# Optimization experiments

Measured on AMD Instinct MI355X. Metric: run time of the kernel, lower is better.

The kernel has to match this reference:

```python
import jax, jax.numpy as jnp
import numpy as np
import math

B, S, D_MODEL, N_HEAD, D_HEAD, D_FFN = 1, 2048, 1024, 16, 64, 4096
EPS = 1e-6


def setup_inputs() -> dict:
    key = jax.random.key(0)
    ks = jax.random.split(key, 10)
    scale = 0.02
    x = jax.random.normal(ks[0], (B, S, D_MODEL), dtype=jnp.float32)
    # RoPE frequencies: freqs_cis[s, i] = exp(1j * s * theta_i), theta_i = 10000^{-2i/d_head}
    half = D_HEAD // 2
    inv_freq = 1.0 / (10000.0 ** (jnp.arange(0, half, dtype=jnp.float32) * 2.0 / D_HEAD))
    angles = jnp.arange(S, dtype=jnp.float32)[:, None] * inv_freq[None, :]  # [S, half]
    freqs_cos = jnp.cos(angles)
    freqs_sin = jnp.sin(angles)
    wq = jax.random.normal(ks[1], (D_MODEL, N_HEAD * D_HEAD), dtype=jnp.float32) * scale
    wk = jax.random.normal(ks[2], (D_MODEL, N_HEAD * D_HEAD), dtype=jnp.float32) * scale
    wv = jax.random.normal(ks[3], (D_MODEL, N_HEAD * D_HEAD), dtype=jnp.float32) * scale
    wo = jax.random.normal(ks[4], (N_HEAD * D_HEAD, D_MODEL), dtype=jnp.float32) * scale
    w1 = jax.random.normal(ks[5], (D_MODEL, D_FFN), dtype=jnp.float32) * scale
    w2 = jax.random.normal(ks[6], (D_FFN, D_MODEL), dtype=jnp.float32) * scale
    w3 = jax.random.normal(ks[7], (D_MODEL, D_FFN), dtype=jnp.float32) * scale
    attn_norm_w = jnp.ones((D_MODEL,), dtype=jnp.float32)
    ffn_norm_w = jnp.ones((D_MODEL,), dtype=jnp.float32)
    return {"x": x, "freqs_cos": freqs_cos, "freqs_sin": freqs_sin,
            "wq": wq, "wk": wk, "wv": wv, "wo": wo,
            "w1": w1, "w2": w2, "w3": w3,
            "attn_norm_w": attn_norm_w, "ffn_norm_w": ffn_norm_w}


def _rmsnorm(x, w):
    xf = x.astype(jnp.float32)
    inv = jax.lax.rsqrt(jnp.mean(xf * xf, axis=-1, keepdims=True) + EPS)
    return (xf * inv).astype(x.dtype) * w


def _rope(t, cos, sin):
    # t: [B, S, H, D]; treat last dim as interleaved (even, odd) complex pairs
    b, s, h, d = t.shape
    tr = t.astype(jnp.float32).reshape(b, s, h, d // 2, 2)
    te, to = tr[..., 0], tr[..., 1]
    c = cos[None, :, None, :]
    sn = sin[None, :, None, :]
    out = jnp.stack([te * c - to * sn, te * sn + to * c], axis=-1)
    return out.reshape(b, s, h, d).astype(t.dtype)


def reference(x, freqs_cos, freqs_sin, wq, wk, wv, wo, w1, w2, w3, attn_norm_w, ffn_norm_w):
    bsz, seqlen, _ = x.shape
    # --- attention sub-block ---
    hin = _rmsnorm(x, attn_norm_w)
    q = (hin @ wq).reshape(bsz, seqlen, N_HEAD, D_HEAD)
    k = (hin @ wk).reshape(bsz, seqlen, N_HEAD, D_HEAD)
    v = (hin @ wv).reshape(bsz, seqlen, N_HEAD, D_HEAD)
    q = _rope(q, freqs_cos, freqs_sin)
    k = _rope(k, freqs_cos, freqs_sin)
    # [B, H, S, S] scores, softmax in fp32 (no causal mask in original)
    scores = jnp.einsum('bqhd,bkhd->bhqk', q, k) / math.sqrt(D_HEAD)
    probs = jax.nn.softmax(scores.astype(jnp.float32), axis=-1).astype(q.dtype)
    attn = jnp.einsum('bhqk,bkhd->bqhd', probs, v).reshape(bsz, seqlen, N_HEAD * D_HEAD)
    h = x + attn @ wo
    # --- SwiGLU FFN sub-block ---
    f = _rmsnorm(h, ffn_norm_w)
    ffn = (jax.nn.silu(f @ w1) * (f @ w3)) @ w2
    return h + ffn
```

## Files before the change

kernel.cpp:

```cpp
#include <hip/hip_runtime.h>
#include <stdint.h>
#include <stddef.h>

using bf16x8 = __attribute__((ext_vector_type(8))) __bf16;
using f32x4  = __attribute__((ext_vector_type(4))) float;
using f32x16 = __attribute__((ext_vector_type(16))) float;

__device__ __forceinline__ float bf2f(unsigned short u) {
  union { unsigned int i; float f; } v; v.i = ((unsigned int)u) << 16; return v.f;
}
__device__ __forceinline__ unsigned short f2bf(float f) {
  union { float f; unsigned int i; } v; v.f = f;
  unsigned int r = v.i + 0x7fffu + ((v.i >> 16) & 1u);
  return (unsigned short)(r >> 16);
}
__device__ __forceinline__ unsigned short f2bf_trunc(float f) {
  union { float f; unsigned int i; } v; v.f = f;
  return (unsigned short)(v.i >> 16);
}
__device__ __forceinline__ unsigned int pk_trunc(float a, float b) {
  union { float f; unsigned int i; } x, y; x.f = a; y.f = b;
  return (x.i >> 16) | (y.i & 0xffff0000u);
}
__device__ __forceinline__ bf16x8 mk_bf16x8(unsigned int a, unsigned int b,
                                            unsigned int c, unsigned int d) {
  union { unsigned int u[4]; bf16x8 v; } x;
  x.u[0] = a; x.u[1] = b; x.u[2] = c; x.u[3] = d; return x.v;
}
__device__ __forceinline__ void async16(const void* g, void* l) {
  __builtin_amdgcn_global_load_lds(
      (const __attribute__((address_space(1))) unsigned int*)g,
      (__attribute__((address_space(3))) unsigned int*)l, 16, 0, 0);
}

#define S_LEN 2048
#define DMODEL 1024
#define NHEAD 16
#define DHEAD 64
#define DFFN 4096

struct PrepArgs {
  const float *wq, *wk, *wv, *wo, *w1, *w3, *w2, *x, *anw;
  unsigned short *WqkvT, *WoT, *W13I, *W2T, *Hin;
};
__global__ __launch_bounds__(256) void prep_k(PrepArgs a) {
  __shared__ unsigned short tile[64][66];
  __shared__ float red[4];
  const int bid = blockIdx.x;
  const int t = threadIdx.x;

  if (bid < 4096) {
    const float* in;
    unsigned short* out;
    int src_ld, dst_ld, bx, by;
    bool w13 = false;
    int rb = 0;
    if (bid < 1024) {
      int z = bid >> 8, rem = bid & 255;
      bx = rem & 15; by = rem >> 4;
      in = z == 0 ? a.wq : z == 1 ? a.wk : z == 2 ? a.wv : a.wo;
      out = z == 0 ? a.WqkvT : z == 1 ? a.WqkvT + 1048576 : z == 2 ? a.WqkvT + 2097152 : a.WoT;
      src_ld = 1024; dst_ld = 1024;
    } else if (bid < 3072) {
      int r = bid - 1024;
      int z = r >> 10, rem = r & 1023;
      bx = rem & 63; by = rem >> 6;
      in = z ? a.w3 : a.w1;
      out = a.W13I;
      src_ld = 4096; dst_ld = 1024;
      w13 = true; rb = z * 32;
    } else {
      int r = bid - 3072;
      bx = r & 15; by = r >> 4;
      in = a.w2; out = a.W2T;
      src_ld = 1024; dst_ld = 4096;
    }
    const int br = by * 64, bc = bx * 64;
    const int rr = t >> 4, c4 = (t & 15) * 4;
#pragma unroll
    for (int i = 0; i < 4; ++i) {
      int row = rr + i * 16;
      float4 v = *(const float4*)&in[(size_t)(br + row) * src_ld + bc + c4];
      tile[row][c4 + 0] = f2bf(v.x);
      tile[row][c4 + 1] = f2bf(v.y);
      tile[row][c4 + 2] = f2bf(v.z);
      tile[row][c4 + 3] = f2bf(v.w);
    }
    __syncthreads();
    const int x = t >> 2, y16 = (t & 3) * 16;
    int dest = bc + x;
    if (w13) dest = (bc >> 5) * 64 + (x >> 5) * 64 + rb + (x & 31);
#pragma unroll
    for (int i = 0; i < 2; ++i) {
      int y0 = y16 + i * 8;
      ushort4 o0, o1;
      o0.x = tile[y0 + 0][x]; o0.y = tile[y0 + 1][x];
      o0.z = tile[y0 + 2][x]; o0.w = tile[y0 + 3][x];
      o1.x = tile[y0 + 4][x]; o1.y = tile[y0 + 5][x];
      o1.z = tile[y0 + 6][x]; o1.w = tile[y0 + 7][x];
      *(ushort4*)&out[(size_t)dest * dst_ld + br + y0] = o0;
      *(ushort4*)&out[(size_t)dest * dst_ld + br + y0 + 4] = o1;
    }
  } else {
    const int row = bid - 4096;
    const int lane = t & 63, w = t >> 6;
    const float* x = a.x + (size_t)row * DMODEL;
    float xs[4];
    float s = 0.f;
#pragma unroll
    for (int i = 0; i < 4; ++i) {
      xs[i] = x[t * 4 + i];
      s += xs[i] * xs[i];
    }
#pragma unroll
    for (int m = 1; m < 64; m <<= 1) s += __shfl_xor(s, m, 64);
    if (lane == 0) red[w] = s;
    __syncthreads();
    float tot = red[0] + red[1] + red[2] + red[3];
    float inv = rsqrtf(tot * (1.0f / DMODEL) + 1e-6f);
#pragma unroll
    for (int i = 0; i < 4; ++i)
      a.Hin[(size_t)row * DMODEL + t * 4 + i] = f2bf(xs[i] * inv * a.anw[t * 4 + i]);
  }
}

__global__ __launch_bounds__(256) void rope_vtrans_k(
    unsigned short* __restrict__ QKV,
    const float* __restrict__ cosp,
    const float* __restrict__ sinp,
    unsigned short* __restrict__ VtG) {
  __shared__ unsigned short tile[64][66];
  const int bid = blockIdx.x;
  const int t = threadIdx.x;
  if (bid < 4096) {
    int idx = bid * 256 + t;
    int s = idx >> 9;
    int rem = idx & 511;
    int h = rem >> 5;
    int i = rem & 31;
    float c = cosp[s * 32 + i];
    float sn = sinp[s * 32 + i];
    size_t off = (size_t)s * 3072 + h * 64 + 2 * i;
    {
      float e = bf2f(QKV[off]), o = bf2f(QKV[off + 1]);
      QKV[off] = f2bf(e * c - o * sn);
      QKV[off + 1] = f2bf(e * sn + o * c);
    }
    {
      float e = bf2f(QKV[off + 1024]), o = bf2f(QKV[off + 1025]);
      QKV[off + 1024] = f2bf((e * c - o * sn) * 0.125f);
      QKV[off + 1025] = f2bf((e * sn + o * c) * 0.125f);
    }
  } else {
    int r = bid - 4096;
    const int bx = r & 15, by = r >> 4;
    const int br = by * 64, bc = bx * 64;
    const int rr = t >> 4, c4 = (t & 15) * 4;
#pragma unroll
    for (int i = 0; i < 4; ++i) {
      int row = rr + i * 16;
      ushort4 v = *(const ushort4*)&QKV[(size_t)(br + row) * 3072 + 2048 + bc + c4];
      tile[row][c4 + 0] = v.x;
      tile[row][c4 + 1] = v.y;
      tile[row][c4 + 2] = v.z;
      tile[row][c4 + 3] = v.w;
    }
    __syncthreads();
    const int x = t >> 2, y16 = (t & 3) * 16;
#pragma unroll
    for (int i = 0; i < 2; ++i) {
      int y0 = y16 + i * 8;
      ushort4 o0, o1;
      o0.x = tile[y0 + 0][x]; o0.y = tile[y0 + 1][x];
      o0.z = tile[y0 + 2][x]; o0.w = tile[y0 + 3][x];
      o1.x = tile[y0 + 4][x]; o1.y = tile[y0 + 5][x];
      o1.z = tile[y0 + 6][x]; o1.w = tile[y0 + 7][x];
      *(ushort4*)&VtG[(size_t)(bc + x) * 2048 + br + y0] = o0;
      *(ushort4*)&VtG[(size_t)(bc + x) * 2048 + br + y0 + 4] = o1;
    }
  }
}

template <int MODE>
__global__ __launch_bounds__(256) void gemm_bt(
    const unsigned short* __restrict__ A, int lda,
    const unsigned short* __restrict__ BT,
    void* __restrict__ Cout,
    int K, int N) {
  __shared__ unsigned short As[128 * 64];
  __shared__ unsigned short Bs[128 * 64];
  const int t = threadIdx.x;
  const int lane = t & 63;
  const int w = t >> 6;
  const int qr = (w >> 1) * 64, qc = (w & 1) * 64;
  const int l31 = lane & 31, half = lane >> 5;
  const int m0 = blockIdx.y * 128, n0 = blockIdx.x * 128;

  f32x16 acc[2][2] = {};

  int srow[4], scol[4];
#pragma unroll
  for (int p = 0; p < 4; ++p) {
    int off = p * 2048 + t * 8;
    int r = off >> 6;
    srow[p] = r;
    scol[p] = ((((off >> 3) & 7) ^ (r & 7) ^ ((r >> 3) & 3))) * 8;
  }
  const int gsw = (l31 & 7) ^ (l31 >> 3);

  for (int k0 = 0; k0 < K; k0 += 64) {
    __syncthreads();
#pragma unroll
    for (int p = 0; p < 4; ++p) {
      int off = p * 2048 + t * 8;
      async16(A + (size_t)(m0 + srow[p]) * lda + (k0 + scol[p]), &As[off]);
      async16(BT + (size_t)(n0 + srow[p]) * K + (k0 + scol[p]), &Bs[off]);
    }
    __syncthreads();
#pragma unroll
    for (int ks = 0; ks < 4; ++ks) {
      const int ch = ((ks * 2 + half) ^ gsw) * 8;
      bf16x8 a0 = *(const bf16x8*)&As[(qr + l31) * 64 + ch];
      bf16x8 a1 = *(const bf16x8*)&As[(qr + 32 + l31) * 64 + ch];
      bf16x8 b0 = *(const bf16x8*)&Bs[(qc + l31) * 64 + ch];
      bf16x8 b1 = *(const bf16x8*)&Bs[(qc + 32 + l31) * 64 + ch];
      acc[0][0] = __builtin_amdgcn_mfma_f32_32x32x16_bf16(a0, b0, acc[0][0], 0, 0, 0);
      acc[0][1] = __builtin_amdgcn_mfma_f32_32x32x16_bf16(a0, b1, acc[0][1], 0, 0, 0);
      acc[1][0] = __builtin_amdgcn_mfma_f32_32x32x16_bf16(a1, b0, acc[1][0], 0, 0, 0);
      acc[1][1] = __builtin_amdgcn_mfma_f32_32x32x16_bf16(a1, b1, acc[1][1], 0, 0, 0);
    }
  }

  {
    unsigned short* C = (unsigned short*)Cout;
#pragma unroll
    for (int rt = 0; rt < 2; ++rt)
#pragma unroll
      for (int ct = 0; ct < 2; ++ct)
#pragma unroll
        for (int reg = 0; reg < 16; ++reg) {
          int rr = m0 + qr + rt * 32 + (reg & 3) + 8 * (reg >> 2) + 4 * half;
          int cc = n0 + qc + ct * 32 + l31;
          C[(size_t)rr * N + cc] = f2bf(acc[rt][ct][reg]);
        }
  }
}

__device__ __forceinline__ void mfma8(f32x16& c0, f32x16& c1,
                                      const bf16x8 (&a)[2][4],
                                      const bf16x8 (&b)[4]) {
  __builtin_amdgcn_s_setprio(1);
#pragma unroll
  for (int ks = 0; ks < 4; ++ks) {
    c0 = __builtin_amdgcn_mfma_f32_32x32x16_bf16(a[0][ks], b[ks], c0, 0, 0, 0);
    c1 = __builtin_amdgcn_mfma_f32_32x32x16_bf16(a[1][ks], b[ks], c1, 0, 0, 0);
  }
  __builtin_amdgcn_s_setprio(0);
}

__global__ __launch_bounds__(512, 2) void gemm256_silu(
    const unsigned short* __restrict__ A,
    const unsigned short* __restrict__ BT,
    unsigned short* __restrict__ F) {
  __shared__ unsigned short lds[65536];
  const int t = threadIdx.x;
  const int l = t & 63, l31 = l & 31, half = l >> 5;
  const int w = t >> 6;
  const int wm = w >> 2, wn = w & 3;

  const int orig = blockIdx.x;
  const int bx = (orig & 7) * 4 + ((orig >> 3) & 3);
  const int by = orig >> 5;
  const int m0 = by * 256, n0 = bx * 256;

  const int rA = t >> 3;
  const int sc = ((t & 7) ^ ((t >> 3) & 7)) * 8;
  const int lo = t * 8;

#define STAGE_A(h, tile, d)                                                    \
  { async16(A + (size_t)(m0 + (h) * 128 + rA) * 1024 + (tile) * 64 + sc,       \
            &lds[(d) * 32768 + (h) * 8192 + lo]);                              \
    async16(A + (size_t)(m0 + (h) * 128 + 64 + rA) * 1024 + (tile) * 64 + sc,  \
            &lds[(d) * 32768 + (h) * 8192 + 4096 + lo]); }
#define STAGE_B(h, tile, d)                                                    \
  { async16(BT + (size_t)(n0 + (h) * 128 + rA) * 1024 + (tile) * 64 + sc,      \
            &lds[(d) * 32768 + 16384 + (h) * 8192 + lo]);                      \
    async16(BT + (size_t)(n0 + (h) * 128 + 64 + rA) * 1024 + (tile) * 64 + sc, \
            &lds[(d) * 32768 + 16384 + (h) * 8192 + 4096 + lo]); }

  const int arow = wm * 128 + l31;
  const int brow = wn * 64 + l31;
  int kc[4];
#pragma unroll
  for (int ks = 0; ks < 4; ++ks) kc[ks] = ((ks * 2 + half) ^ (l31 & 7)) * 8;

#define LDA(d, mt, ks) (*(const bf16x8*)&lds[(d) * 32768 + (arow + (mt) * 32) * 64 + kc[ks]])
#define LDB(d, nt, ks) (*(const bf16x8*)&lds[(d) * 32768 + 16384 + (brow + (nt) * 32) * 64 + kc[ks]])

  f32x16 acc[4][2] = {};
  bf16x8 afr[2][4], bfr[2][4];

  STAGE_A(0, 0, 0); STAGE_A(1, 0, 0); STAGE_B(0, 0, 0); STAGE_B(1, 0, 0);
  STAGE_A(0, 1, 1); STAGE_A(1, 1, 1);
  asm volatile("s_waitcnt vmcnt(4)" ::: "memory");
  __builtin_amdgcn_s_barrier();

#pragma unroll 1
  for (int i = 0; i < 8; ++i) {
    const int t1 = 2 * i + 1, t2 = 2 * i + 2, t3 = 2 * i + 3;
    const bool more = i < 7;

#pragma unroll
    for (int ks = 0; ks < 4; ++ks) {
      afr[0][ks] = LDA(0, 0, ks);
      afr[1][ks] = LDA(0, 1, ks);
      bfr[0][ks] = LDB(0, 0, ks);
    }
    STAGE_B(0, t1, 1);
    __builtin_amdgcn_s_barrier();
    mfma8(acc[0][0], acc[1][0], afr, bfr[0]);
    __builtin_amdgcn_s_barrier();

#pragma unroll
    for (int ks = 0; ks < 4; ++ks) bfr[1][ks] = LDB(0, 1, ks);
    STAGE_B(1, t1, 1);
    __builtin_amdgcn_s_barrier();
    mfma8(acc[0][1], acc[1][1], afr, bfr[1]);
    __builtin_amdgcn_s_barrier();

#pragma unroll
    for (int ks = 0; ks < 4; ++ks) {
      afr[0][ks] = LDA(0, 2, ks);
      afr[1][ks] = LDA(0, 3, ks);
    }
    if (more) STAGE_B(0, t2, 0);
    __builtin_amdgcn_s_barrier();
    mfma8(acc[2][1], acc[3][1], afr, bfr[1]);
    __builtin_amdgcn_s_barrier();

    if (more) {
      STAGE_B(1, t2, 0);
      STAGE_A(0, t2, 0);
      asm volatile("s_waitcnt vmcnt(8)" ::: "memory");
    } else {
      asm volatile("s_waitcnt vmcnt(2)" ::: "memory");
    }
    __builtin_amdgcn_s_barrier();
    mfma8(acc[2][0], acc[3][0], afr, bfr[0]);
    __builtin_amdgcn_s_barrier();

#pragma unroll
    for (int ks = 0; ks < 4; ++ks) {
      afr[0][ks] = LDA(1, 0, ks);
      afr[1][ks] = LDA(1, 1, ks);
      bfr[0][ks] = LDB(1, 0, ks);
    }
    if (more) {
      STAGE_A(1, t2, 0);
      asm volatile("s_waitcnt vmcnt(8)" ::: "memory");
    } else {
      asm volatile("s_waitcnt vmcnt(0)" ::: "memory");
    }
    __builtin_amdgcn_s_barrier();
    mfma8(acc[0][0], acc[1][0], afr, bfr[0]);
    __builtin_amdgcn_s_barrier();

#pragma unroll
    for (int ks = 0; ks < 4; ++ks) bfr[1][ks] = LDB(1, 1, ks);
    __builtin_amdgcn_s_barrier();
    mfma8(acc[0][1], acc[1][1], afr, bfr[1]);
    __builtin_amdgcn_s_barrier();

#pragma unroll
    for (int ks = 0; ks < 4; ++ks) {
      afr[0][ks] = LDA(1, 2, ks);
      afr[1][ks] = LDA(1, 3, ks);
    }
    __builtin_amdgcn_s_barrier();
    mfma8(acc[2][1], acc[3][1], afr, bfr[1]);
    __builtin_amdgcn_s_barrier();

    if (more) {
      STAGE_A(0, t3, 1);
      STAGE_A(1, t3, 1);
      asm volatile("s_waitcnt vmcnt(4)" ::: "memory");
    } else {
      asm volatile("s_waitcnt vmcnt(0)" ::: "memory");
    }
    __builtin_amdgcn_s_barrier();
    mfma8(acc[2][0], acc[3][0], afr, bfr[0]);
    __builtin_amdgcn_s_barrier();
  }

#undef STAGE_A
#undef STAGE_B
#undef LDA
#undef LDB

  const int ccol = (n0 >> 1) + wn * 32 + l31;
  const int rbase = m0 + wm * 128 + 4 * half;
#pragma unroll
  for (int mt = 0; mt < 4; ++mt)
#pragma unroll
    for (int reg = 0; reg < 16; ++reg) {
      int rr = rbase + mt * 32 + (reg & 3) + 8 * (reg >> 2);
      float a1v = acc[mt][0][reg];
      float a3v = acc[mt][1][reg];
      float f = a1v / (1.f + __expf(-a1v)) * a3v;
      F[(size_t)rr * 4096 + ccol] = f2bf(f);
    }
}

struct PtrPair { float* p0; float* p1; };

__global__ __launch_bounds__(256) void gemm_bt_sk2(
    const unsigned short* __restrict__ A, int lda,
    const unsigned short* __restrict__ BT,
    PtrPair parts, int Kc, int Ktot, int N) {
  __shared__ unsigned short As[128 * 64];
  __shared__ unsigned short Bs[128 * 64];
  const int t = threadIdx.x;
  const int lane = t & 63;
  const int w = t >> 6;
  const int qr = (w >> 1) * 64, qc = (w & 1) * 64;
  const int l31 = lane & 31, half = lane >> 5;
  const int m0 = blockIdx.y * 128, n0 = blockIdx.x * 128;
  const int kb = blockIdx.z * Kc;

  f32x16 acc[2][2] = {};

  int srow[4], scol[4];
#pragma unroll
  for (int p = 0; p < 4; ++p) {
    int off = p * 2048 + t * 8;
    int r = off >> 6;
    srow[p] = r;
    scol[p] = ((((off >> 3) & 7) ^ (r & 7) ^ ((r >> 3) & 3))) * 8;
  }
  const int gsw = (l31 & 7) ^ (l31 >> 3);

  for (int k0 = kb; k0 < kb + Kc; k0 += 64) {
    __syncthreads();
#pragma unroll
    for (int p = 0; p < 4; ++p) {
      int off = p * 2048 + t * 8;
      async16(A + (size_t)(m0 + srow[p]) * lda + (k0 + scol[p]), &As[off]);
      async16(BT + (size_t)(n0 + srow[p]) * Ktot + (k0 + scol[p]), &Bs[off]);
    }
    __syncthreads();
#pragma unroll
    for (int ks = 0; ks < 4; ++ks) {
      const int ch = ((ks * 2 + half) ^ gsw) * 8;
      bf16x8 a0 = *(const bf16x8*)&As[(qr + l31) * 64 + ch];
      bf16x8 a1 = *(const bf16x8*)&As[(qr + 32 + l31) * 64 + ch];
      bf16x8 b0 = *(const bf16x8*)&Bs[(qc + l31) * 64 + ch];
      bf16x8 b1 = *(const bf16x8*)&Bs[(qc + 32 + l31) * 64 + ch];
      acc[0][0] = __builtin_amdgcn_mfma_f32_32x32x16_bf16(a0, b0, acc[0][0], 0, 0, 0);
      acc[0][1] = __builtin_amdgcn_mfma_f32_32x32x16_bf16(a0, b1, acc[0][1], 0, 0, 0);
      acc[1][0] = __builtin_amdgcn_mfma_f32_32x32x16_bf16(a1, b0, acc[1][0], 0, 0, 0);
      acc[1][1] = __builtin_amdgcn_mfma_f32_32x32x16_bf16(a1, b1, acc[1][1], 0, 0, 0);
    }
  }

  float* C = blockIdx.z ? parts.p1 : parts.p0;
#pragma unroll
  for (int rt = 0; rt < 2; ++rt)
#pragma unroll
    for (int ct = 0; ct < 2; ++ct)
#pragma unroll
      for (int reg = 0; reg < 16; ++reg) {
        int rr = m0 + qr + rt * 32 + (reg & 3) + 8 * (reg >> 2) + 4 * half;
        int cc = n0 + qc + ct * 32 + l31;
        C[(size_t)rr * N + cc] = acc[rt][ct][reg];
      }
}

__global__ __launch_bounds__(256) void reduce2_k(
    const float4* __restrict__ P0, const float4* __restrict__ P1,
    const float4* __restrict__ R, float4* __restrict__ Out, int nvec) {
  int i = blockIdx.x * 256 + threadIdx.x;
  if (i >= nvec) return;
  float4 a = P0[i], b = P1[i], r = R[i];
  float4 o;
  o.x = a.x + b.x + r.x;
  o.y = a.y + b.y + r.y;
  o.z = a.z + b.z + r.z;
  o.w = a.w + b.w + r.w;
  Out[i] = o;
}

__global__ __launch_bounds__(256) void reduce_norm_k(
    const float4* __restrict__ P0, const float4* __restrict__ P1,
    const float4* __restrict__ R, float4* __restrict__ Hres,
    const float* __restrict__ W, unsigned short* __restrict__ Hin) {
  const int row = blockIdx.x;
  const int t = threadIdx.x;
  const int lane = t & 63, w = t >> 6;
  const int i = row * 256 + t;
  float4 a = P0[i], b = P1[i], r = R[i];
  float4 h;
  h.x = a.x + b.x + r.x;
  h.y = a.y + b.y + r.y;
  h.z = a.z + b.z + r.z;
  h.w = a.w + b.w + r.w;
  Hres[i] = h;
  float s = h.x * h.x + h.y * h.y + h.z * h.z + h.w * h.w;
#pragma unroll
  for (int m = 1; m < 64; m <<= 1) s += __shfl_xor(s, m, 64);
  __shared__ float red[4];
  if (lane == 0) red[w] = s;
  __syncthreads();
  float tot = red[0] + red[1] + red[2] + red[3];
  float inv = rsqrtf(tot * (1.0f / DMODEL) + 1e-6f);
  ushort4 o;
  o.x = f2bf(h.x * inv * W[t * 4 + 0]);
  o.y = f2bf(h.y * inv * W[t * 4 + 1]);
  o.z = f2bf(h.z * inv * W[t * 4 + 2]);
  o.w = f2bf(h.w * inv * W[t * 4 + 3]);
  *(ushort4*)(Hin + (size_t)row * DMODEL + t * 4) = o;
}

__global__ __launch_bounds__(256) void attn_k(
    const unsigned short* __restrict__ QKV,
    const unsigned short* __restrict__ VtG,
    float* __restrict__ O0, float* __restrict__ O1,
    float* __restrict__ L) {
  const int h = blockIdx.y;
  const int qb = blockIdx.x;
  const int z = blockIdx.z;
  const int t = threadIdx.x;
  const int lane = t & 63;
  const int l31 = lane & 31, half = lane >> 5;
  const int w = t >> 6;
  const int q0 = qb * 128 + w * 32;
  const int kbase = z * 1024;
  const int gsw = (l31 & 7) ^ (l31 >> 3);

  __shared__ unsigned short Kt[2][64 * 64];
  __shared__ unsigned short Vt[2][64 * 64];

  const unsigned short* Kp = QKV + 1024 + h * 64;
  const unsigned short* Vg = VtG + (size_t)h * 64 * 2048;

  bf16x8 qf[4];
#pragma unroll
  for (int ks = 0; ks < 4; ++ks)
    qf[ks] = *(const bf16x8*)(QKV + (size_t)(q0 + l31) * 3072 + h * 64 + ks * 16 + half * 8);

#pragma unroll
  for (int p = 0; p < 2; ++p) {
    int off = p * 2048 + t * 8;
    int r = off >> 6;
    int sc8 = (((off >> 3) & 7) ^ (r & 7) ^ ((r >> 3) & 3)) * 8;
    async16(Kp + (size_t)(kbase + r) * 3072 + sc8, &Kt[0][off]);
    async16(Vg + (size_t)r * 2048 + kbase + sc8, &Vt[0][off]);
  }
  asm volatile("s_waitcnt vmcnt(0)" ::: "memory");
  __syncthreads();

  f32x16 oacc[2] = {};
  float l_r = 0.f;

#pragma unroll 1
  for (int kt = 0; kt < 16; ++kt) {
    const int cur = kt & 1;
    if (kt + 1 < 16) {
      int kb2 = kbase + (kt + 1) * 64;
#pragma unroll
      for (int p = 0; p < 2; ++p) {
        int off = p * 2048 + t * 8;
        int r = off >> 6;
        int sc8 = (((off >> 3) & 7) ^ (r & 7) ^ ((r >> 3) & 3)) * 8;
        async16(Kp + (size_t)(kb2 + r) * 3072 + sc8, &Kt[cur ^ 1][off]);
        async16(Vg + (size_t)r * 2048 + kb2 + sc8, &Vt[cur ^ 1][off]);
      }
    }

    f32x16 st[2] = {};
#pragma unroll
    for (int ks = 0; ks < 4; ++ks) {
      const int ch = ((2 * ks + half) ^ gsw) * 8;
      bf16x8 k0 = *(const bf16x8*)&Kt[cur][l31 * 64 + ch];
      bf16x8 k1 = *(const bf16x8*)&Kt[cur][(32 + l31) * 64 + ch];
      st[0] = __builtin_amdgcn_mfma_f32_32x32x16_bf16(k0, qf[ks], st[0], 0, 0, 0);
      st[1] = __builtin_amdgcn_mfma_f32_32x32x16_bf16(k1, qf[ks], st[1], 0, 0, 0);
    }

    float psum = 0.f;
#pragma unroll
    for (int b = 0; b < 2; ++b)
#pragma unroll
      for (int r = 0; r < 16; ++r) {
        float e = __expf(st[b][r]);
        st[b][r] = e;
        psum += e;
      }
    l_r += psum;

    unsigned int pklo[8], pkhi[8];
#pragma unroll
    for (int b = 0; b < 2; ++b)
#pragma unroll
      for (int m = 0; m < 4; ++m) {
        pklo[b * 4 + m] = pk_trunc(st[b][4 * m + 0], st[b][4 * m + 1]);
        pkhi[b * 4 + m] = pk_trunc(st[b][4 * m + 2], st[b][4 * m + 3]);
      }

#pragma unroll
    for (int ks = 0; ks < 4; ++ks) {
      unsigned int keep_lo = half ? pklo[2 * ks + 1] : pklo[2 * ks];
      unsigned int keep_hi = half ? pkhi[2 * ks + 1] : pkhi[2 * ks];
      unsigned int pass_lo = half ? pklo[2 * ks] : pklo[2 * ks + 1];
      unsigned int pass_hi = half ? pkhi[2 * ks] : pkhi[2 * ks + 1];
      unsigned int olo = (unsigned int)__shfl_xor((int)pass_lo, 32, 64);
      unsigned int ohi = (unsigned int)__shfl_xor((int)pass_hi, 32, 64);
      unsigned int w0 = half ? olo : keep_lo;
      unsigned int w1 = half ? ohi : keep_hi;
      unsigned int w2 = half ? keep_lo : olo;
      unsigned int w3 = half ? keep_hi : ohi;
      bf16x8 af = mk_bf16x8(w0, w1, w2, w3);
      const int ch = ((2 * ks + half) ^ gsw) * 8;
      bf16x8 v0 = *(const bf16x8*)&Vt[cur][l31 * 64 + ch];
      bf16x8 v1 = *(const bf16x8*)&Vt[cur][(32 + l31) * 64 + ch];
      oacc[0] = __builtin_amdgcn_mfma_f32_32x32x16_bf16(af, v0, oacc[0], 0, 0, 0);
      oacc[1] = __builtin_amdgcn_mfma_f32_32x32x16_bf16(af, v1, oacc[1], 0, 0, 0);
    }

    __syncthreads();
  }

  float lt = l_r + __shfl_xor(l_r, 32, 64);
  float* Op = z ? O1 : O0;
#pragma unroll
  for (int db = 0; db < 2; ++db)
#pragma unroll
    for (int reg = 0; reg < 16; ++reg) {
      int q = (reg & 3) + 8 * (reg >> 2) + 4 * half;
      Op[(size_t)(q0 + q) * DMODEL + h * 64 + db * 32 + l31] = oacc[db][reg];
    }
  if (half == 0)
    L[(size_t)(h * 2 + z) * S_LEN + q0 + l31] = lt;
}

__global__ __launch_bounds__(256) void attn_combine_k(
    const float4* __restrict__ O0, const float4* __restrict__ O1,
    const float* __restrict__ L, unsigned short* __restrict__ Attn) {
  int i = blockIdx.x * 256 + threadIdx.x;
  int e0 = i * 4;
  int s = e0 >> 10;
  int c = e0 & 1023;
  int h = c >> 6;
  float la = L[(size_t)(h * 2) * S_LEN + s];
  float lb = L[(size_t)(h * 2 + 1) * S_LEN + s];
  float inv = 1.f / (la + lb);
  float4 a = O0[i], b = O1[i];
  ushort4 r;
  r.x = f2bf((a.x + b.x) * inv);
  r.y = f2bf((a.y + b.y) * inv);
  r.z = f2bf((a.z + b.z) * inv);
  r.w = f2bf((a.w + b.w) * inv);
  *(ushort4*)(Attn + e0) = r;
}

extern "C" void kernel_launch(void* const* d_in, const int* in_sizes, int n_in,
                              void* d_out, int out_size, void* d_ws, size_t ws_size,
                              hipStream_t stream) {
  (void)in_sizes; (void)n_in; (void)out_size; (void)ws_size;
  const float* x    = (const float*)d_in[0];
  const float* fcos = (const float*)d_in[1];
  const float* fsin = (const float*)d_in[2];
  const float* wq   = (const float*)d_in[3];
  const float* wk   = (const float*)d_in[4];
  const float* wv   = (const float*)d_in[5];
  const float* wo   = (const float*)d_in[6];
  const float* w1   = (const float*)d_in[7];
  const float* w2   = (const float*)d_in[8];
  const float* w3   = (const float*)d_in[9];
  const float* anw  = (const float*)d_in[10];
  const float* fnw  = (const float*)d_in[11];
  float* out = (float*)d_out;
  char* ws = (char*)d_ws;

  unsigned short* WqkvT = (unsigned short*)(ws + 0);
  unsigned short* VtG   = (unsigned short*)(ws + 0);
  float*          Lbuf  = (float*)(ws + 4194304);
  unsigned short* WoT   = (unsigned short*)(ws + 6291456);
  unsigned short* QKV   = (unsigned short*)(ws + 8388608);
  unsigned short* Attn  = (unsigned short*)(ws + 20971520);
  float* Oa             = (float*)(ws + 25165824);
  float* Ob             = (float*)(ws + 37748736);
  float* P0a            = (float*)(ws + 8388608);
  float* P1a            = (float*)(ws + 25165824);
  unsigned short* F     = (unsigned short*)(ws + 0);
  float* P0b            = (float*)(ws + 16777216);
  float* P1b            = (float*)(ws + 25165824);
  unsigned short* Hin   = (unsigned short*)(ws + 33554432);
  float*          Hres  = (float*)        (ws + 37748736);
  unsigned short* W13I  = (unsigned short*)(ws + 46137344);
  unsigned short* W2T   = (unsigned short*)(ws + 62914560);

  prep_k<<<6144, 256, 0, stream>>>(PrepArgs{
      wq, wk, wv, wo, w1, w3, w2, x, anw,
      WqkvT, WoT, W13I, W2T, Hin});

  gemm_bt<0><<<dim3(24, 16), 256, 0, stream>>>(Hin, 1024, WqkvT, QKV, 1024, 3072);
  rope_vtrans_k<<<4608, 256, 0, stream>>>(QKV, fcos, fsin, VtG);
  attn_k<<<dim3(16, 16, 2), 256, 0, stream>>>(QKV, VtG, Oa, Ob, Lbuf);
  attn_combine_k<<<2048, 256, 0, stream>>>((const float4*)Oa, (const float4*)Ob, Lbuf, Attn);
  gemm_bt_sk2<<<dim3(8, 16, 2), 256, 0, stream>>>(Attn, 1024, WoT, PtrPair{P0a, P1a}, 512, 1024, 1024);
  reduce_norm_k<<<2048, 256, 0, stream>>>((const float4*)P0a, (const float4*)P1a,
                                          (const float4*)x, (float4*)Hres, fnw, Hin);

  gemm256_silu<<<dim3(256), 512, 0, stream>>>(Hin, W13I, F);
  gemm_bt_sk2<<<dim3(8, 16, 2), 256, 0, stream>>>(F, 4096, W2T, PtrPair{P0b, P1b}, 2048, 4096, 1024);
  reduce2_k<<<2048, 256, 0, stream>>>((const float4*)P0b, (const float4*)P1b,
                                      (const float4*)Hres, (float4*)out, 524288);
}
```

Baseline: 288.4 us.

## Replace split-K attention plus combine with single-pass 64-query-block attention

Drops the two-way split over the key dimension and the separate combine kernel. Each 128-thread block now handles 64 queries over all 2048 keys and writes normalized bf16 output directly. This removes the fp32 partial-output round trip through memory and one kernel launch. In exchange, each block runs a longer serial loop and each K/V tile loaded into shared memory is reused by half as many queries, so K/V traffic per query rises. Grid size stays at 512 blocks, but each block now has half the threads.

```diff
diff --git a/kernel.cpp b/kernel.cpp
--- a/kernel.cpp
+++ b/kernel.cpp
@@ -520,20 +520,17 @@
   *(ushort4*)(Hin + (size_t)row * DMODEL + t * 4) = o;
 }
 
-__global__ __launch_bounds__(256) void attn_k(
+__global__ __launch_bounds__(128) void attn2_k(
     const unsigned short* __restrict__ QKV,
     const unsigned short* __restrict__ VtG,
-    float* __restrict__ O0, float* __restrict__ O1,
-    float* __restrict__ L) {
+    unsigned short* __restrict__ Attn) {
   const int h = blockIdx.y;
   const int qb = blockIdx.x;
-  const int z = blockIdx.z;
   const int t = threadIdx.x;
   const int lane = t & 63;
   const int l31 = lane & 31, half = lane >> 5;
   const int w = t >> 6;
-  const int q0 = qb * 128 + w * 32;
-  const int kbase = z * 1024;
+  const int q0 = qb * 64 + w * 32;
   const int gsw = (l31 & 7) ^ (l31 >> 3);
 
   __shared__ unsigned short Kt[2][64 * 64];
@@ -548,12 +545,12 @@
     qf[ks] = *(const bf16x8*)(QKV + (size_t)(q0 + l31) * 3072 + h * 64 + ks * 16 + half * 8);
 
 #pragma unroll
-  for (int p = 0; p < 2; ++p) {
-    int off = p * 2048 + t * 8;
+  for (int p = 0; p < 4; ++p) {
+    int off = p * 1024 + t * 8;
     int r = off >> 6;
     int sc8 = (((off >> 3) & 7) ^ (r & 7) ^ ((r >> 3) & 3)) * 8;
-    async16(Kp + (size_t)(kbase + r) * 3072 + sc8, &Kt[0][off]);
-    async16(Vg + (size_t)r * 2048 + kbase + sc8, &Vt[0][off]);
+    async16(Kp + (size_t)r * 3072 + sc8, &Kt[0][off]);
+    async16(Vg + (size_t)r * 2048 + sc8, &Vt[0][off]);
   }
   asm volatile("s_waitcnt vmcnt(0)" ::: "memory");
   __syncthreads();
@@ -562,13 +559,13 @@
   float l_r = 0.f;
 
 #pragma unroll 1
-  for (int kt = 0; kt < 16; ++kt) {
+  for (int kt = 0; kt < 32; ++kt) {
     const int cur = kt & 1;
-    if (kt + 1 < 16) {
-      int kb2 = kbase + (kt + 1) * 64;
-#pragma unroll
-      for (int p = 0; p < 2; ++p) {
-        int off = p * 2048 + t * 8;
+    if (kt + 1 < 32) {
+      int kb2 = (kt + 1) * 64;
+#pragma unroll
+      for (int p = 0; p < 4; ++p) {
+        int off = p * 1024 + t * 8;
         int r = off >> 6;
         int sc8 = (((off >> 3) & 7) ^ (r & 7) ^ ((r >> 3) & 3)) * 8;
         async16(Kp + (size_t)(kb2 + r) * 3072 + sc8, &Kt[cur ^ 1][off]);
@@ -630,36 +627,15 @@
   }
 
   float lt = l_r + __shfl_xor(l_r, 32, 64);
-  float* Op = z ? O1 : O0;
+  float inv = 1.f / lt;
 #pragma unroll
   for (int db = 0; db < 2; ++db)
 #pragma unroll
     for (int reg = 0; reg < 16; ++reg) {
       int q = (reg & 3) + 8 * (reg >> 2) + 4 * half;
-      Op[(size_t)(q0 + q) * DMODEL + h * 64 + db * 32 + l31] = oacc[db][reg];
-    }
-  if (half == 0)
-    L[(size_t)(h * 2 + z) * S_LEN + q0 + l31] = lt;
-}
-
-__global__ __launch_bounds__(256) void attn_combine_k(
-    const float4* __restrict__ O0, const float4* __restrict__ O1,
-    const float* __restrict__ L, unsigned short* __restrict__ Attn) {
-  int i = blockIdx.x * 256 + threadIdx.x;
-  int e0 = i * 4;
-  int s = e0 >> 10;
-  int c = e0 & 1023;
-  int h = c >> 6;
-  float la = L[(size_t)(h * 2) * S_LEN + s];
-  float lb = L[(size_t)(h * 2 + 1) * S_LEN + s];
-  float inv = 1.f / (la + lb);
-  float4 a = O0[i], b = O1[i];
-  ushort4 r;
-  r.x = f2bf((a.x + b.x) * inv);
-  r.y = f2bf((a.y + b.y) * inv);
-  r.z = f2bf((a.z + b.z) * inv);
-  r.w = f2bf((a.w + b.w) * inv);
-  *(ushort4*)(Attn + e0) = r;
+      Attn[(size_t)(q0 + q) * DMODEL + h * 64 + db * 32 + l31] =
+          f2bf(oacc[db][reg] * inv);
+    }
 }
 
 extern "C" void kernel_launch(void* const* d_in, const int* in_sizes, int n_in,
@@ -683,12 +659,9 @@
 
   unsigned short* WqkvT = (unsigned short*)(ws + 0);
   unsigned short* VtG   = (unsigned short*)(ws + 0);
-  float*          Lbuf  = (float*)(ws + 4194304);
   unsigned short* WoT   = (unsigned short*)(ws + 6291456);
   unsigned short* QKV   = (unsigned short*)(ws + 8388608);
   unsigned short* Attn  = (unsigned short*)(ws + 20971520);
-  float* Oa             = (float*)(ws + 25165824);
-  float* Ob             = (float*)(ws + 37748736);
   float* P0a            = (float*)(ws + 8388608);
   float* P1a            = (float*)(ws + 25165824);
   unsigned short* F     = (unsigned short*)(ws + 0);
@@ -705,8 +678,7 @@
 
   gemm_bt<0><<<dim3(24, 16), 256, 0, stream>>>(Hin, 1024, WqkvT, QKV, 1024, 3072);
   rope_vtrans_k<<<4608, 256, 0, stream>>>(QKV, fcos, fsin, VtG);
-  attn_k<<<dim3(16, 16, 2), 256, 0, stream>>>(QKV, VtG, Oa, Ob, Lbuf);
-  attn_combine_k<<<2048, 256, 0, stream>>>((const float4*)Oa, (const float4*)Ob, Lbuf, Attn);
+  attn2_k<<<dim3(32, 16), 128, 0, stream>>>(QKV, VtG, Attn);
   gemm_bt_sk2<<<dim3(8, 16, 2), 256, 0, stream>>>(Attn, 1024, WoT, PtrPair{P0a, P1a}, 512, 1024, 1024);
   reduce_norm_k<<<2048, 256, 0, stream>>>((const float4*)P0a, (const float4*)P1a,
                                           (const float4*)x, (float4*)Hres, fnw, Hin);
```

After: 304.5 us. 5.6% more time.

## Accumulate W2 split-K partials atomically into output, dropping the reduce kernel

Applied to the files above, without the earlier changes.

The FFN down-projection now splits K four ways instead of two and has each split atomically add its fp32 tile straight into the output buffer. The output is pre-seeded with the residual h by the norm kernel, so the separate partial buffers and the reduce2 kernel go away. This removes one launch and the write-then-reread of two partial tensors, and doubles the block count for better CU occupancy. The cost is contended fp32 atomics and non-deterministic summation order. The MFMA ordering in the silu GEMM's last two steps is also swapped, which is likely a scheduling tweak.

```diff
diff --git a/kernel.cpp b/kernel.cpp
--- a/kernel.cpp
+++ b/kernel.cpp
@@ -335,7 +335,7 @@
     }
     if (more) STAGE_B(0, t2, 0);
     __builtin_amdgcn_s_barrier();
-    mfma8(acc[2][1], acc[3][1], afr, bfr[1]);
+    mfma8(acc[2][0], acc[3][0], afr, bfr[0]);
     __builtin_amdgcn_s_barrier();
 
     if (more) {
@@ -346,7 +346,7 @@
       asm volatile("s_waitcnt vmcnt(2)" ::: "memory");
     }
     __builtin_amdgcn_s_barrier();
-    mfma8(acc[2][0], acc[3][0], afr, bfr[0]);
+    mfma8(acc[2][1], acc[3][1], afr, bfr[1]);
     __builtin_amdgcn_s_barrier();
 
 #pragma unroll
@@ -377,7 +377,7 @@
       afr[1][ks] = LDA(1, 3, ks);
     }
     __builtin_amdgcn_s_barrier();
-    mfma8(acc[2][1], acc[3][1], afr, bfr[1]);
+    mfma8(acc[2][0], acc[3][0], afr, bfr[0]);
     __builtin_amdgcn_s_barrier();
 
     if (more) {
@@ -388,7 +388,7 @@
       asm volatile("s_waitcnt vmcnt(0)" ::: "memory");
     }
     __builtin_amdgcn_s_barrier();
-    mfma8(acc[2][0], acc[3][0], afr, bfr[0]);
+    mfma8(acc[2][1], acc[3][1], afr, bfr[1]);
     __builtin_amdgcn_s_barrier();
   }
 
@@ -413,10 +413,11 @@
 
 struct PtrPair { float* p0; float* p1; };
 
-__global__ __launch_bounds__(256) void gemm_bt_sk2(
+template <bool ATOMIC>
+__device__ __forceinline__ void gemm_sk_body(
     const unsigned short* __restrict__ A, int lda,
     const unsigned short* __restrict__ BT,
-    PtrPair parts, int Kc, int Ktot, int N) {
+    float* __restrict__ C, int Kc, int Ktot, int N, int kb) {
   __shared__ unsigned short As[128 * 64];
   __shared__ unsigned short Bs[128 * 64];
   const int t = threadIdx.x;
@@ -425,7 +426,6 @@
   const int qr = (w >> 1) * 64, qc = (w & 1) * 64;
   const int l31 = lane & 31, half = lane >> 5;
   const int m0 = blockIdx.y * 128, n0 = blockIdx.x * 128;
-  const int kb = blockIdx.z * Kc;
 
   f32x16 acc[2][2] = {};
 
@@ -462,7 +462,6 @@
     }
   }
 
-  float* C = blockIdx.z ? parts.p1 : parts.p0;
 #pragma unroll
   for (int rt = 0; rt < 2; ++rt)
 #pragma unroll
@@ -471,27 +470,31 @@
       for (int reg = 0; reg < 16; ++reg) {
         int rr = m0 + qr + rt * 32 + (reg & 3) + 8 * (reg >> 2) + 4 * half;
         int cc = n0 + qc + ct * 32 + l31;
-        C[(size_t)rr * N + cc] = acc[rt][ct][reg];
+        if constexpr (ATOMIC)
+          atomicAdd(&C[(size_t)rr * N + cc], acc[rt][ct][reg]);
+        else
+          C[(size_t)rr * N + cc] = acc[rt][ct][reg];
       }
 }
 
-__global__ __launch_bounds__(256) void reduce2_k(
-    const float4* __restrict__ P0, const float4* __restrict__ P1,
-    const float4* __restrict__ R, float4* __restrict__ Out, int nvec) {
-  int i = blockIdx.x * 256 + threadIdx.x;
-  if (i >= nvec) return;
-  float4 a = P0[i], b = P1[i], r = R[i];
-  float4 o;
-  o.x = a.x + b.x + r.x;
-  o.y = a.y + b.y + r.y;
-  o.z = a.z + b.z + r.z;
-  o.w = a.w + b.w + r.w;
-  Out[i] = o;
+__global__ __launch_bounds__(256) void gemm_bt_sk2(
+    const unsigned short* __restrict__ A, int lda,
+    const unsigned short* __restrict__ BT,
+    PtrPair parts, int Kc, int Ktot, int N) {
+  float* C = blockIdx.z ? parts.p1 : parts.p0;
+  gemm_sk_body<false>(A, lda, BT, C, Kc, Ktot, N, blockIdx.z * Kc);
+}
+
+__global__ __launch_bounds__(256) void gemm_bt_sk4a(
+    const unsigned short* __restrict__ A, int lda,
+    const unsigned short* __restrict__ BT,
+    float* __restrict__ Out, int Kc, int Ktot, int N) {
+  gemm_sk_body<true>(A, lda, BT, Out, Kc, Ktot, N, blockIdx.z * Kc);
 }
 
 __global__ __launch_bounds__(256) void reduce_norm_k(
     const float4* __restrict__ P0, const float4* __restrict__ P1,
-    const float4* __restrict__ R, float4* __restrict__ Hres,
+    const float4* __restrict__ R, float4* __restrict__ Out,
     const float* __restrict__ W, unsigned short* __restrict__ Hin) {
   const int row = blockIdx.x;
   const int t = threadIdx.x;
@@ -503,7 +506,7 @@
   h.y = a.y + b.y + r.y;
   h.z = a.z + b.z + r.z;
   h.w = a.w + b.w + r.w;
-  Hres[i] = h;
+  Out[i] = h;
   float s = h.x * h.x + h.y * h.y + h.z * h.z + h.w * h.w;
 #pragma unroll
   for (int m = 1; m < 64; m <<= 1) s += __shfl_xor(s, m, 64);
@@ -692,10 +695,7 @@
   float* P0a            = (float*)(ws + 8388608);
   float* P1a            = (float*)(ws + 25165824);
   unsigned short* F     = (unsigned short*)(ws + 0);
-  float* P0b            = (float*)(ws + 16777216);
-  float* P1b            = (float*)(ws + 25165824);
   unsigned short* Hin   = (unsigned short*)(ws + 33554432);
-  float*          Hres  = (float*)        (ws + 37748736);
   unsigned short* W13I  = (unsigned short*)(ws + 46137344);
   unsigned short* W2T   = (unsigned short*)(ws + 62914560);
 
@@ -709,10 +709,8 @@
   attn_combine_k<<<2048, 256, 0, stream>>>((const float4*)Oa, (const float4*)Ob, Lbuf, Attn);
   gemm_bt_sk2<<<dim3(8, 16, 2), 256, 0, stream>>>(Attn, 1024, WoT, PtrPair{P0a, P1a}, 512, 1024, 1024);
   reduce_norm_k<<<2048, 256, 0, stream>>>((const float4*)P0a, (const float4*)P1a,
-                                          (const float4*)x, (float4*)Hres, fnw, Hin);
+                                          (const float4*)x, (float4*)out, fnw, Hin);
 
   gemm256_silu<<<dim3(256), 512, 0, stream>>>(Hin, W13I, F);
-  gemm_bt_sk2<<<dim3(8, 16, 2), 256, 0, stream>>>(F, 4096, W2T, PtrPair{P0b, P1b}, 2048, 4096, 1024);
-  reduce2_k<<<2048, 256, 0, stream>>>((const float4*)P0b, (const float4*)P1b,
-                                      (const float4*)Hres, (float4*)out, 524288);
-}
+  gemm_bt_sk4a<<<dim3(8, 16, 4), 256, 0, stream>>>(F, 4096, W2T, out, 1024, 4096, 1024);
+}
```

After: 298.6 us. 1.04x slower.
